# Kernel optimization log

Hardware: AMD Instinct MI355X
Metric: run time of the kernel (lower is better)

## Reference

```python
import jax, jax.numpy as jnp
import numpy as np

A, B, O, ACT, H, NH = 16, 8192, 128, 16, 128, 4
D = H // NH  # attend_dim
IN = O + ACT
NEG = -1e9


def setup_inputs() -> dict:
    key = jax.random.key(0)
    ks = jax.random.split(key, 16)
    s = lambda k, shape, fan: jax.random.normal(k, shape, jnp.float32) / np.sqrt(fan)
    return {
        "obs": jax.random.normal(ks[0], (A, B, O), jnp.float32),
        "actions": jax.random.uniform(ks[1], (A, B, ACT), jnp.float32),
        # per-agent sa-encoder (enc_fc1)
        "W_sa": s(ks[2], (A, IN, H), IN), "b_sa": jnp.zeros((A, H), jnp.float32),
        # per-agent state encoder (s_enc_fc1)
        "W_s": s(ks[3], (A, O, H), O), "b_s": jnp.zeros((A, H), jnp.float32),
        # shared per-head extractors
        "Wk": s(ks[4], (NH, H, D), H),
        "Wsel": s(ks[5], (NH, H, D), H),
        "Wv": s(ks[6], (NH, H, D), H), "bv": jnp.zeros((NH, D), jnp.float32),
        # per-agent critic MLP
        "Wc1": s(ks[7], (A, 2 * H, H), 2 * H), "bc1": jnp.zeros((A, H), jnp.float32),
        "Wc2": s(ks[8], (A, H, ACT), H), "bc2": jnp.zeros((A, ACT), jnp.float32),
    }


def _bn(x):
    # BatchNorm1d(affine=False) in training mode: normalize over batch axis, biased var
    m = x.mean(axis=1, keepdims=True)
    v = x.var(axis=1, keepdims=True)
    return (x - m) / jnp.sqrt(v + 1e-5)


def reference(obs, actions, W_sa, b_sa, W_s, b_s, Wk, Wsel, Wv, bv, Wc1, bc1, Wc2, bc2):
    lrelu = jax.nn.leaky_relu  # slope 0.01, matches torch default
    inp = jnp.concatenate([obs, actions], axis=-1)            # [A,B,IN]
    sa = lrelu(jnp.einsum('abi,aih->abh', _bn(inp), W_sa) + b_sa[:, None, :])  # [A,B,H]
    se = lrelu(jnp.einsum('abo,aoh->abh', _bn(obs), W_s) + b_s[:, None, :])    # [A,B,H]
    keys = jnp.einsum('abh,nhd->nabd', sa, Wk)                # [NH,A,B,D]
    vals = lrelu(jnp.einsum('abh,nhd->nabd', sa, Wv) + bv[:, None, None, :])
    sel = jnp.einsum('abh,nhd->nabd', se, Wsel)
    logits = jnp.einsum('nibd,njbd->nibj', sel, keys) / np.sqrt(D)  # [NH,A,B,A]
    self_mask = jnp.eye(A, dtype=bool)[None, :, None, :]      # mask j == i
    w = jax.nn.softmax(jnp.where(self_mask, NEG, logits), axis=-1)
    other = jnp.einsum('nibj,njbd->nibd', w, vals)            # [NH,A,B,D]
    other = jnp.transpose(other, (1, 2, 0, 3)).reshape(A, B, NH * D)  # head-order concat
    cin = jnp.concatenate([se, other], axis=-1)               # [A,B,2H]
    h = lrelu(jnp.einsum('abk,akh->abh', cin, Wc1) + bc1[:, None, :])
    all_q = jnp.einsum('abh,aho->abo', h, Wc2) + bc2[:, None, :]      # [A,B,ACT]
    idx = jnp.argmax(actions, axis=-1)[..., None]             # int_acs, [A,B,1]
    q = jnp.take_along_axis(all_q, idx, axis=-1)              # [A,B,1]
    return q
```

## Files before the change

### kernel.cpp

```cpp
#include <hip/hip_runtime.h>
#include <hip/hip_bf16.h>

#define A_N 16
#define B_N 8192
#define O_N 128
#define ACT_N 16
#define H_N 128
#define NH_N 4
#define D_N 32
#define IN_N 144
#define NEGV -1e9f

typedef __attribute__((ext_vector_type(8))) short short8;
typedef __attribute__((ext_vector_type(4))) float floatx4;

static __device__ inline unsigned short f2bf(float f) {
    union { float f; unsigned u; } x{f};
    unsigned u = x.u + 0x7FFFu + ((x.u >> 16) & 1u);
    return (unsigned short)(u >> 16);
}
static __device__ inline unsigned pack_bf2(float a, float b) {
    union { float f; unsigned u; } xa{a}, xb{b};
    unsigned ua = xa.u + 0x7FFFu + ((xa.u >> 16) & 1u);
    unsigned ub = xb.u + 0x7FFFu + ((xb.u >> 16) & 1u);
    return (ua >> 16) | (ub & 0xFFFF0000u);
}
static __device__ inline float bf2f(unsigned short h) {
    union { unsigned u; float f; } x;
    x.u = ((unsigned)h) << 16;
    return x.f;
}
static __device__ inline float bflo(unsigned u) {
    union { unsigned u; float f; } x; x.u = u << 16; return x.f;
}
static __device__ inline float bfhi(unsigned u) {
    union { unsigned u; float f; } x; x.u = u & 0xFFFF0000u; return x.f;
}
static __device__ inline short8 ld_frag(const unsigned* p) {
    union { unsigned u[4]; short8 v; } x;
    uint2 lo = *(const uint2*)p;
    uint2 hi = *(const uint2*)(p + 2);
    x.u[0] = lo.x; x.u[1] = lo.y; x.u[2] = hi.x; x.u[3] = hi.y;
    return x.v;
}
static __device__ inline short8 ld_frag4(const unsigned* p) {
    union { uint4 q; short8 v; } x;
    x.q = *(const uint4*)p;
    return x.v;
}

__global__ __launch_bounds__(256) void k_zero(float* p, int n) {
    int i = blockIdx.x * 256 + threadIdx.x;
    if (i < n) p[i] = 0.f;
}

__global__ __launch_bounds__(256) void k_stats(const float* __restrict__ obs,
                                               const float* __restrict__ act,
                                               float* __restrict__ gsum,
                                               float* __restrict__ gsq) {
    __shared__ float ssum[IN_N];
    __shared__ float ssq[IN_N];
    int a = blockIdx.x >> 4;
    int r0 = (blockIdx.x & 15) * 512;
    int t = threadIdx.x;
    if (t < IN_N) { ssum[t] = 0.f; ssq[t] = 0.f; }
    __syncthreads();
    {
        int c0 = (t & 31) * 4, rg = t >> 5;
        const float* p = obs + ((size_t)a * B_N + r0 + rg) * O_N + c0;
        float s0 = 0.f, s1 = 0.f, s2 = 0.f, s3 = 0.f;
        float q0 = 0.f, q1 = 0.f, q2 = 0.f, q3 = 0.f;
#pragma unroll 4
        for (int i = 0; i < 64; ++i) {
            float4 v = *(const float4*)(p + (size_t)i * 8 * O_N);
            s0 += v.x; q0 += v.x * v.x;
            s1 += v.y; q1 += v.y * v.y;
            s2 += v.z; q2 += v.z * v.z;
            s3 += v.w; q3 += v.w * v.w;
        }
        atomicAdd(&ssum[c0 + 0], s0); atomicAdd(&ssq[c0 + 0], q0);
        atomicAdd(&ssum[c0 + 1], s1); atomicAdd(&ssq[c0 + 1], q1);
        atomicAdd(&ssum[c0 + 2], s2); atomicAdd(&ssq[c0 + 2], q2);
        atomicAdd(&ssum[c0 + 3], s3); atomicAdd(&ssq[c0 + 3], q3);
    }
    if (t < 128) {
        int f = t & 15, rg = t >> 4;
        const float* p = act + ((size_t)a * B_N + r0 + rg) * ACT_N + f;
        float s = 0.f, q = 0.f;
#pragma unroll 4
        for (int i = 0; i < 64; ++i) {
            float v = p[(size_t)i * 8 * ACT_N];
            s += v; q += v * v;
        }
        atomicAdd(&ssum[O_N + f], s);
        atomicAdd(&ssq[O_N + f], q);
    }
    __syncthreads();
    if (t < IN_N) {
        atomicAdd(&gsum[a * IN_N + t], ssum[t]);
        atomicAdd(&gsq[a * IN_N + t], ssq[t]);
    }
}

__global__ __launch_bounds__(256) void k_finalize(float* gsum, float* gsq) {
    int i = blockIdx.x * 256 + threadIdx.x;
    if (i < A_N * IN_N) {
        const float invB = 1.f / (float)B_N;
        float m = gsum[i] * invB;
        float v = fmaxf(gsq[i] * invB - m * m, 0.f);
        gsum[i] = m;
        gsq[i] = rsqrtf(v + 1e-5f);
    }
}

#define L1E 393216
#define P1E 409600
#define P2E 417792
#define CRE 679936
#define C2E 712704
__global__ __launch_bounds__(256) void k_wprep(
    const float* __restrict__ W_sa, const float* __restrict__ W_s,
    const float* __restrict__ Wk, const float* __restrict__ Wsel,
    const float* __restrict__ Wv, const float* __restrict__ Wc1,
    const float* __restrict__ Wc2, const float* __restrict__ rstd,
    unsigned* __restrict__ wt_l1, unsigned* __restrict__ wt_p1,
    unsigned* __restrict__ wt_p2, unsigned* __restrict__ wt_cr,
    float* __restrict__ wt_c2) {
    int idx = blockIdx.x * 256 + threadIdx.x;
    if (idx < L1E) {
        int a = idx / 24576, rem = idx % 24576;
        int n = rem & 255, kp = rem >> 8;
        int k0 = 2 * kp, k1 = k0 + 1;
        float v0 = 0.f, v1 = 0.f;
        if (n < 128) {
            if (k0 < IN_N) v0 = W_sa[((size_t)a * IN_N + k0) * H_N + n] * rstd[a * IN_N + k0];
            if (k1 < IN_N) v1 = W_sa[((size_t)a * IN_N + k1) * H_N + n] * rstd[a * IN_N + k1];
        } else {
            int m = n - 128;
            if (k0 < O_N) v0 = W_s[((size_t)a * O_N + k0) * H_N + m] * rstd[a * IN_N + k0];
            if (k1 < O_N) v1 = W_s[((size_t)a * O_N + k1) * H_N + m] * rstd[a * IN_N + k1];
        }
        wt_l1[(size_t)a * 24576 + n * 96 + kp] = pack_bf2(v0, v1);
    } else if (idx < P1E) {
        int i2 = idx - L1E;
        int n = i2 & 255, kp = i2 >> 8;
        int k0 = 2 * kp;
        float v0, v1;
        if (n < 128) {
            const float* w = Wk + ((size_t)(n >> 5) * H_N) * D_N + (n & 31);
            v0 = w[(size_t)k0 * D_N]; v1 = w[(size_t)(k0 + 1) * D_N];
        } else {
            int m = n - 128;
            const float* w = Wv + ((size_t)(m >> 5) * H_N) * D_N + (m & 31);
            v0 = w[(size_t)k0 * D_N]; v1 = w[(size_t)(k0 + 1) * D_N];
        }
        wt_p1[n * 64 + kp] = pack_bf2(v0, v1);
    } else if (idx < P2E) {
        int i3 = idx - P1E;
        int n = i3 & 127, kp = i3 >> 7;
        int k0 = 2 * kp;
        const float* w = Wsel + ((size_t)(n >> 5) * H_N) * D_N + (n & 31);
        wt_p2[n * 64 + kp] = pack_bf2(w[(size_t)k0 * D_N], w[(size_t)(k0 + 1) * D_N]);
    } else if (idx < CRE) {
        int i4 = idx - P2E;
        int a = i4 >> 14, r = i4 & 16383;
        int n = r & 127, kp = r >> 7;
        int k0 = 2 * kp;
        const float* w = Wc1 + (size_t)a * 256 * H_N + n;
        wt_cr[(size_t)a * 16384 + n * 128 + kp] =
            pack_bf2(w[(size_t)k0 * H_N], w[(size_t)(k0 + 1) * H_N]);
    } else if (idx < C2E) {
        int i5 = idx - CRE;
        int a = i5 >> 11, rem = i5 & 2047;
        int oo = rem >> 7, h = rem & 127;
        wt_c2[i5] = Wc2[((size_t)a * H_N + h) * ACT_N + oo];
    }
}

__global__ __launch_bounds__(256) void k_bfold(
    const float* __restrict__ mean, const float* __restrict__ rstd,
    const float* __restrict__ W_sa, const float* __restrict__ W_s,
    const float* __restrict__ b_sa, const float* __restrict__ b_s,
    float* __restrict__ fb) {
    int a = blockIdx.x, c = threadIdx.x;
    float s = 0.f;
    if (c < 128) {
        for (int k = 0; k < IN_N; ++k)
            s += mean[a * IN_N + k] * rstd[a * IN_N + k] *
                 W_sa[((size_t)a * IN_N + k) * H_N + c];
        fb[a * 128 + c] = b_sa[a * H_N + c] - s;
    } else {
        int m = c - 128;
        for (int k = 0; k < O_N; ++k)
            s += mean[a * IN_N + k] * rstd[a * IN_N + k] *
                 W_s[((size_t)a * O_N + k) * H_N + m];
        fb[2048 + a * 128 + m] = b_s[a * H_N + m] - s;
    }
}

__global__ __launch_bounds__(512, 2) void k_l1(
    const float* __restrict__ obs, const float* __restrict__ act,
    const unsigned* __restrict__ wt_l1, const float* __restrict__ fb,
    unsigned short* __restrict__ sa_us, unsigned short* __restrict__ se_us,
    int b0g, int Bc) {
    __shared__ unsigned smem[(128 + 256) * 34];
    unsigned* Xs = smem;
    unsigned* Ws = smem + 128 * 34;

    int a = blockIdx.y;
    int b0 = blockIdx.x * 128;
    int t = threadIdx.x;
    int wid = t >> 6, lane = t & 63, lm = lane & 15, lq = lane >> 4;
    int wrow = (wid & 1) * 64;
    int wcol = (wid >> 1) * 64;

    floatx4 acc[4][4];
#pragma unroll
    for (int mt = 0; mt < 4; ++mt)
#pragma unroll
        for (int nt = 0; nt < 4; ++nt)
#pragma unroll
            for (int e = 0; e < 4; ++e) acc[mt][nt][e] = 0.f;

    const unsigned* WtA = wt_l1 + (size_t)a * 24576;

    for (int c = 0; c < 3; ++c) {
        int kk = c * 64;
        __syncthreads();
        for (int idx = t; idx < 128 * 16; idx += 512) {
            int r = idx >> 4, c4 = idx & 15;
            int k = kk + c4 * 4;
            size_t grow = (size_t)a * B_N + b0g + b0 + r;
            float4 v;
            if (k < O_N) v = *(const float4*)&obs[grow * O_N + k];
            else if (k < IN_N) v = *(const float4*)&act[grow * ACT_N + (k - O_N)];
            else v = make_float4(0.f, 0.f, 0.f, 0.f);
            uint2* dst = (uint2*)&Xs[r * 34 + c4 * 2];
            *dst = make_uint2(pack_bf2(v.x, v.y), pack_bf2(v.z, v.w));
        }
        for (int idx = t; idx < 256 * 8; idx += 512) {
            int n = idx >> 3, c4 = idx & 7;
            uint4 w = *(const uint4*)&WtA[(size_t)n * 96 + (kk >> 1) + c4 * 4];
            uint2* dst = (uint2*)&Ws[n * 34 + c4 * 4];
            dst[0] = make_uint2(w.x, w.y);
            dst[1] = make_uint2(w.z, w.w);
        }
        __syncthreads();
#pragma unroll
        for (int s = 0; s < 2; ++s) {
            if (kk + s * 32 >= 160) break;
            short8 afr[4];
#pragma unroll
            for (int mt = 0; mt < 4; ++mt)
                afr[mt] = ld_frag(&Xs[(wrow + mt * 16 + lm) * 34 + s * 16 + lq * 4]);
#pragma unroll
            for (int nt = 0; nt < 4; ++nt) {
                short8 bfr = ld_frag(&Ws[(wcol + nt * 16 + lm) * 34 + s * 16 + lq * 4]);
#pragma unroll
                for (int mt = 0; mt < 4; ++mt)
                    acc[mt][nt] = __builtin_amdgcn_mfma_f32_16x16x32_bf16(
                        afr[mt], bfr, acc[mt][nt], 0, 0, 0);
            }
        }
    }

    int zsel = (wcol >= 128);
    unsigned short* outp = zsel ? se_us : sa_us;
    const float* bias = fb + zsel * 2048 + a * 128;
    int cbase = wcol & 127;
#pragma unroll
    for (int mt = 0; mt < 4; ++mt)
#pragma unroll
        for (int nt = 0; nt < 4; ++nt)
#pragma unroll
            for (int r = 0; r < 4; ++r) {
                int row = wrow + mt * 16 + lq * 4 + r;
                int col = cbase + nt * 16 + lm;
                float v = acc[mt][nt][r] + bias[col];
                v = v > 0.f ? v : 0.01f * v;
                outp[((size_t)(b0 + row) * 16 + a) * 128 + col] = f2bf(v);
            }
}

__global__ __launch_bounds__(256, 3) void k_fused(
    const unsigned* __restrict__ sa_u, const unsigned* __restrict__ se_u,
    const unsigned* __restrict__ wt_p1, const unsigned* __restrict__ wt_p2,
    const float* __restrict__ bv, unsigned short* __restrict__ other_us,
    int Bc) {
    __shared__ unsigned short keys_s[64 * 130];
    __shared__ unsigned short vals_s[64 * 136];
    __shared__ unsigned short sel_s[64 * 132];

    int bg0 = blockIdx.x * 4;
    int t = threadIdx.x;
    int wid = t >> 6, lane = t & 63, lm = lane & 15, lq = lane >> 4;

    const unsigned* sa_base = sa_u + (size_t)(bg0 * 16) * 64;
    const unsigned* se_base = se_u + (size_t)(bg0 * 16) * 64;

    {
        floatx4 acc[4][4];
#pragma unroll
        for (int mt = 0; mt < 4; ++mt)
#pragma unroll
            for (int nt = 0; nt < 4; ++nt)
#pragma unroll
                for (int e = 0; e < 4; ++e) acc[mt][nt][e] = 0.f;
#pragma unroll
        for (int s = 0; s < 4; ++s) {
            short8 afr[4];
#pragma unroll
            for (int mt = 0; mt < 4; ++mt)
                afr[mt] = ld_frag4(sa_base + (size_t)(mt * 16 + lm) * 64 + s * 16 + lq * 4);
#pragma unroll
            for (int nt = 0; nt < 4; ++nt) {
                int col = wid * 64 + nt * 16 + lm;
                short8 bfr = ld_frag4(wt_p1 + (size_t)col * 64 + s * 16 + lq * 4);
#pragma unroll
                for (int mt = 0; mt < 4; ++mt)
                    acc[mt][nt] = __builtin_amdgcn_mfma_f32_16x16x32_bf16(
                        afr[mt], bfr, acc[mt][nt], 0, 0, 0);
            }
        }
        if (wid < 2) {
#pragma unroll
            for (int mt = 0; mt < 4; ++mt)
#pragma unroll
                for (int nt = 0; nt < 4; ++nt)
#pragma unroll
                    for (int r = 0; r < 4; ++r) {
                        int row = mt * 16 + lq * 4 + r;
                        int col = wid * 64 + nt * 16 + lm;
                        keys_s[row * 130 + col] = f2bf(acc[mt][nt][r]);
                    }
        } else {
#pragma unroll
            for (int mt = 0; mt < 4; ++mt)
#pragma unroll
                for (int nt = 0; nt < 4; ++nt) {
                    int col = (wid - 2) * 64 + nt * 16 + lm;
                    float bvc = bv[col];
#pragma unroll
                    for (int r = 0; r < 4; ++r) {
                        int row = mt * 16 + lq * 4 + r;
                        float v = acc[mt][nt][r] + bvc;
                        v = v > 0.f ? v : 0.01f * v;
                        vals_s[row * 136 + col] = f2bf(v);
                    }
                }
        }
    }
    __syncthreads();

    {
        int wcol = wid * 32;
        floatx4 acc[4][2];
#pragma unroll
        for (int mt = 0; mt < 4; ++mt)
#pragma unroll
            for (int nt = 0; nt < 2; ++nt)
#pragma unroll
                for (int e = 0; e < 4; ++e) acc[mt][nt][e] = 0.f;
#pragma unroll
        for (int s = 0; s < 4; ++s) {
            short8 afr[4];
#pragma unroll
            for (int mt = 0; mt < 4; ++mt)
                afr[mt] = ld_frag4(se_base + (size_t)(mt * 16 + lm) * 64 + s * 16 + lq * 4);
#pragma unroll
            for (int nt = 0; nt < 2; ++nt) {
                int col = wcol + nt * 16 + lm;
                short8 bfr = ld_frag4(wt_p2 + (size_t)col * 64 + s * 16 + lq * 4);
#pragma unroll
                for (int mt = 0; mt < 4; ++mt)
                    acc[mt][nt] = __builtin_amdgcn_mfma_f32_16x16x32_bf16(
                        afr[mt], bfr, acc[mt][nt], 0, 0, 0);
            }
        }
#pragma unroll
        for (int mt = 0; mt < 4; ++mt)
#pragma unroll
            for (int nt = 0; nt < 2; ++nt)
#pragma unroll
                for (int r = 0; r < 4; ++r) {
                    int row = mt * 16 + lq * 4 + r;
                    int col = wcol + nt * 16 + lm;
                    sel_s[row * 132 + col] = f2bf(acc[mt][nt][r]);
                }
    }
    __syncthreads();

    const unsigned* selU = (const unsigned*)sel_s;
    const unsigned* keysU = (const unsigned*)keys_s;
    floatx4 lgacc[4];
#pragma unroll
    for (int n = 0; n < 4; ++n) {
        short8 af = ld_frag(&selU[(wid * 16 + lm) * 66 + n * 16 + lq * 4]);
        short8 bf = ld_frag(&keysU[(wid * 16 + lm) * 65 + n * 16 + lq * 4]);
        floatx4 z4 = {0.f, 0.f, 0.f, 0.f};
        lgacc[n] = __builtin_amdgcn_mfma_f32_16x16x32_bf16(af, bf, z4, 0, 0, 0);
    }
    __syncthreads();

    float* lgs = (float*)keys_s;
#pragma unroll
    for (int n = 0; n < 4; ++n)
#pragma unroll
        for (int r = 0; r < 4; ++r) {
            int i = lq * 4 + r;
            lgs[((wid * 4 + n) * 16 + i) * 16 + lm] =
                lgacc[n][r] * 0.17677669529663687f;
        }
    asm volatile("" ::: "memory");

    int bsub = wid, n = (t >> 4) & 3, i = t & 15;
    float lg[16];
    {
        const float4* lgp = (const float4*)&lgs[((bsub * 4 + n) * 16 + i) * 16];
#pragma unroll
        for (int c = 0; c < 4; ++c) {
            float4 v = lgp[c];
            lg[4 * c] = v.x; lg[4 * c + 1] = v.y;
            lg[4 * c + 2] = v.z; lg[4 * c + 3] = v.w;
        }
    }
    lg[i] = NEGV;
    float m = lg[0];
#pragma unroll
    for (int j = 1; j < 16; ++j) m = fmaxf(m, lg[j]);
    float sum = 0.f;
#pragma unroll
    for (int j = 0; j < 16; ++j) { lg[j] = __expf(lg[j] - m); sum += lg[j]; }
    float inv = 1.f / sum;
#pragma unroll
    for (int j = 0; j < 16; ++j) lg[j] *= inv;

    const unsigned* valsU = (const unsigned*)vals_s;
    float ov[32];
#pragma unroll
    for (int u = 0; u < 32; ++u) ov[u] = 0.f;
#pragma unroll
    for (int j = 0; j < 16; ++j) {
        const uint4* vrow = (const uint4*)&valsU[(bsub * 16 + j) * 68 + n * 16];
        float w = lg[j];
#pragma unroll
        for (int c = 0; c < 4; ++c) {
            uint4 x = vrow[c];
            ov[8 * c + 0] = fmaf(w, bflo(x.x), ov[8 * c + 0]);
            ov[8 * c + 1] = fmaf(w, bfhi(x.x), ov[8 * c + 1]);
            ov[8 * c + 2] = fmaf(w, bflo(x.y), ov[8 * c + 2]);
            ov[8 * c + 3] = fmaf(w, bfhi(x.y), ov[8 * c + 3]);
            ov[8 * c + 4] = fmaf(w, bflo(x.z), ov[8 * c + 4]);
            ov[8 * c + 5] = fmaf(w, bfhi(x.z), ov[8 * c + 5]);
            ov[8 * c + 6] = fmaf(w, bflo(x.w), ov[8 * c + 6]);
            ov[8 * c + 7] = fmaf(w, bfhi(x.w), ov[8 * c + 7]);
        }
    }
    {
        uint4* orow = (uint4*)&other_us[((size_t)(bg0 + bsub) * 16 + i) * 128 + n * 32];
#pragma unroll
        for (int h = 0; h < 2; ++h) {
            uint4 o;
            o.x = pack_bf2(ov[16 * h + 0], ov[16 * h + 1]);
            o.y = pack_bf2(ov[16 * h + 2], ov[16 * h + 3]);
            o.z = pack_bf2(ov[16 * h + 4], ov[16 * h + 5]);
            o.w = pack_bf2(ov[16 * h + 6], ov[16 * h + 7]);
            orow[2 * h] = o;
            o.x = pack_bf2(ov[16 * h + 8], ov[16 * h + 9]);
            o.y = pack_bf2(ov[16 * h + 10], ov[16 * h + 11]);
            o.z = pack_bf2(ov[16 * h + 12], ov[16 * h + 13]);
            o.w = pack_bf2(ov[16 * h + 14], ov[16 * h + 15]);
            orow[2 * h + 1] = o;
        }
    }
}

__global__ __launch_bounds__(256, 4) void k_critic(
    const unsigned* __restrict__ se_u, const unsigned* __restrict__ other_u,
    const unsigned* __restrict__ wt_cr,
    const float* __restrict__ bc1, const float* __restrict__ actions,
    const float* __restrict__ wt_c2, const float* __restrict__ bc2,
    float* __restrict__ qout, int b0g, int Bc) {
    __shared__ unsigned smem[(64 + 128) * 34];
    unsigned* Xs = smem;
    unsigned* Ws = smem + 64 * 34;

    int a = blockIdx.y;
    int b0 = blockIdx.x * 64;
    int t = threadIdx.x;
    int wid = t >> 6, lane = t & 63, lm = lane & 15, lq = lane >> 4;
    int wrow = (wid & 1) * 32;
    int wcol = (wid >> 1) * 64;

    floatx4 acc[2][4];
#pragma unroll
    for (int mt = 0; mt < 2; ++mt)
#pragma unroll
        for (int nt = 0; nt < 4; ++nt)
#pragma unroll
            for (int e = 0; e < 4; ++e) acc[mt][nt][e] = 0.f;

    const unsigned* WtA = wt_cr + (size_t)a * 16384;

    for (int c = 0; c < 4; ++c) {
        int kk = c * 64;
        __syncthreads();
        const unsigned* src = (c < 2) ? se_u : other_u;
        int off = (c & 1) * 32;
        for (int idx = t; idx < 64 * 8; idx += 256) {
            int r = idx >> 3, c4 = idx & 7;
            uint4 v = *(const uint4*)&src[((size_t)(b0 + r) * 16 + a) * 64 + off + c4 * 4];
            uint2* dst = (uint2*)&Xs[r * 34 + c4 * 4];
            dst[0] = make_uint2(v.x, v.y);
            dst[1] = make_uint2(v.z, v.w);
        }
        for (int idx = t; idx < 128 * 8; idx += 256) {
            int n = idx >> 3, c4 = idx & 7;
            uint4 w = *(const uint4*)&WtA[(size_t)n * 128 + (kk >> 1) + c4 * 4];
            uint2* dst = (uint2*)&Ws[n * 34 + c4 * 4];
            dst[0] = make_uint2(w.x, w.y);
            dst[1] = make_uint2(w.z, w.w);
        }
        __syncthreads();
#pragma unroll
        for (int s = 0; s < 2; ++s) {
            short8 afr[2];
#pragma unroll
            for (int mt = 0; mt < 2; ++mt)
                afr[mt] = ld_frag(&Xs[(wrow + mt * 16 + lm) * 34 + s * 16 + lq * 4]);
#pragma unroll
            for (int nt = 0; nt < 4; ++nt) {
                short8 bfr = ld_frag(&Ws[(wcol + nt * 16 + lm) * 34 + s * 16 + lq * 4]);
#pragma unroll
                for (int mt = 0; mt < 2; ++mt)
                    acc[mt][nt] = __builtin_amdgcn_mfma_f32_16x16x32_bf16(
                        afr[mt], bfr, acc[mt][nt], 0, 0, 0);
            }
        }
    }

    __syncthreads();
    unsigned short* hbuf = (unsigned short*)smem;
#pragma unroll
    for (int mt = 0; mt < 2; ++mt)
#pragma unroll
        for (int nt = 0; nt < 4; ++nt)
#pragma unroll
            for (int r = 0; r < 4; ++r) {
                int row = wrow + mt * 16 + lq * 4 + r;
                int col = wcol + nt * 16 + lm;
                float v = acc[mt][nt][r] + bc1[a * H_N + col];
                v = v > 0.f ? v : 0.01f * v;
                hbuf[row * 132 + col] = f2bf(v);
            }
    __syncthreads();
    if (t < 64) {
        size_t arow = (size_t)a * B_N + b0g + b0 + t;
        const float* ap = &actions[arow * ACT_N];
        float bestv = ap[0];
        int bi = 0;
        for (int o = 1; o < ACT_N; ++o) {
            float v = ap[o];
            if (v > bestv) { bestv = v; bi = o; }
        }
        float q = bc2[a * ACT_N + bi];
        const float4* w4p = (const float4*)&wt_c2[((size_t)a * ACT_N + bi) * H_N];
        const uint2* hp2 = (const uint2*)&hbuf[t * 132];
#pragma unroll
        for (int h4 = 0; h4 < 32; ++h4) {
            float4 w4 = w4p[h4];
            uint2 hh = hp2[h4];
            q = fmaf(bflo(hh.x), w4.x, q);
            q = fmaf(bfhi(hh.x), w4.y, q);
            q = fmaf(bflo(hh.y), w4.z, q);
            q = fmaf(bfhi(hh.y), w4.w, q);
        }
        qout[arow] = q;
    }
}

extern "C" void kernel_launch(void* const* d_in, const int* in_sizes, int n_in,
                              void* d_out, int out_size, void* d_ws, size_t ws_size,
                              hipStream_t stream) {
    const float* obs     = (const float*)d_in[0];
    const float* actions = (const float*)d_in[1];
    const float* W_sa    = (const float*)d_in[2];
    const float* b_sa    = (const float*)d_in[3];
    const float* W_s     = (const float*)d_in[4];
    const float* b_s     = (const float*)d_in[5];
    const float* Wk      = (const float*)d_in[6];
    const float* Wsel    = (const float*)d_in[7];
    const float* Wv      = (const float*)d_in[8];
    const float* bv      = (const float*)d_in[9];
    const float* Wc1     = (const float*)d_in[10];
    const float* bc1     = (const float*)d_in[11];
    const float* Wc2     = (const float*)d_in[12];
    const float* bc2     = (const float*)d_in[13];
    float* out = (float*)d_out;
    char* ws = (char*)d_ws;

    size_t o = 0;
    float* gsum = (float*)(ws + o); o += 2304 * 4;
    float* gsq  = (float*)(ws + o); o += 2304 * 4;
    unsigned* wt_l1 = (unsigned*)(ws + o); o += (size_t)393216 * 4;
    unsigned* wt_p1 = (unsigned*)(ws + o); o += (size_t)16384 * 4;
    unsigned* wt_p2 = (unsigned*)(ws + o); o += (size_t)8192 * 4;
    unsigned* wt_cr = (unsigned*)(ws + o); o += (size_t)262144 * 4;
    float* fb = (float*)(ws + o); o += (size_t)4096 * 4;
    float* wt_c2 = (float*)(ws + o); o += (size_t)32768 * 4;
    size_t fixed = o;

    int Bc = B_N;
    while (Bc > 128 && fixed + 12288ull * Bc > ws_size) Bc >>= 1;

    unsigned short* sa_us = (unsigned short*)(ws + o); o += (size_t)A_N * Bc * 128 * 2;
    unsigned short* se_us = (unsigned short*)(ws + o); o += (size_t)A_N * Bc * 128 * 2;
    unsigned short* ot_us = (unsigned short*)(ws + o); o += (size_t)A_N * Bc * 128 * 2;

    k_zero<<<dim3(18), 256, 0, stream>>>(gsum, 2 * A_N * IN_N);
    k_stats<<<dim3(A_N * 16), 256, 0, stream>>>(obs, actions, gsum, gsq);
    k_finalize<<<dim3(9), 256, 0, stream>>>(gsum, gsq);
    k_wprep<<<dim3(C2E / 256), 256, 0, stream>>>(W_sa, W_s, Wk, Wsel, Wv, Wc1, Wc2,
                                                 gsq, wt_l1, wt_p1, wt_p2, wt_cr, wt_c2);
    k_bfold<<<dim3(A_N), 256, 0, stream>>>(gsum, gsq, W_sa, W_s, b_sa, b_s, fb);

    for (int b0g = 0; b0g < B_N; b0g += Bc) {
        k_l1<<<dim3(Bc / 128, A_N), 512, 0, stream>>>(
            obs, actions, wt_l1, fb, sa_us, se_us, b0g, Bc);
        k_fused<<<dim3(Bc / 4), 256, 0, stream>>>(
            (const unsigned*)sa_us, (const unsigned*)se_us, wt_p1, wt_p2, bv,
            ot_us, Bc);
        k_critic<<<dim3(Bc / 64, A_N), 256, 0, stream>>>(
            (const unsigned*)se_us, (const unsigned*)ot_us, wt_cr, bc1,
            actions, wt_c2, bc2, out, b0g, Bc);
    }
}
```

Baseline: 299.4 us.

## Drop zero/bfold launches, stage tiles in LDS, move attention softmax-V onto MFMA

```diff
diff --git a/kernel.cpp b/kernel.cpp
--- a/kernel.cpp
+++ b/kernel.cpp
@@ -49,19 +49,15 @@
     return x.v;
 }
 
-__global__ __launch_bounds__(256) void k_zero(float* p, int n) {
-    int i = blockIdx.x * 256 + threadIdx.x;
-    if (i < n) p[i] = 0.f;
-}
-
 __global__ __launch_bounds__(256) void k_stats(const float* __restrict__ obs,
                                                const float* __restrict__ act,
-                                               float* __restrict__ gsum,
-                                               float* __restrict__ gsq) {
+                                               float* __restrict__ gsumP,
+                                               float* __restrict__ gsqP) {
     __shared__ float ssum[IN_N];
     __shared__ float ssq[IN_N];
     int a = blockIdx.x >> 4;
-    int r0 = (blockIdx.x & 15) * 512;
+    int slab = blockIdx.x & 15;
+    int r0 = slab * 512;
     int t = threadIdx.x;
     if (t < IN_N) { ssum[t] = 0.f; ssq[t] = 0.f; }
     __syncthreads();
@@ -97,19 +93,29 @@
     }
     __syncthreads();
     if (t < IN_N) {
-        atomicAdd(&gsum[a * IN_N + t], ssum[t]);
-        atomicAdd(&gsq[a * IN_N + t], ssq[t]);
-    }
-}
-
-__global__ __launch_bounds__(256) void k_finalize(float* gsum, float* gsq) {
+        gsumP[(a * 16 + slab) * IN_N + t] = ssum[t];
+        gsqP[(a * 16 + slab) * IN_N + t] = ssq[t];
+    }
+}
+
+__global__ __launch_bounds__(256) void k_finalize(const float* __restrict__ gsumP,
+                                                  const float* __restrict__ gsqP,
+                                                  float* __restrict__ mean,
+                                                  float* __restrict__ rstd) {
     int i = blockIdx.x * 256 + threadIdx.x;
     if (i < A_N * IN_N) {
+        int a = i / IN_N, f = i - a * IN_N;
+        float s = 0.f, q = 0.f;
+#pragma unroll
+        for (int sl = 0; sl < 16; ++sl) {
+            s += gsumP[(a * 16 + sl) * IN_N + f];
+            q += gsqP[(a * 16 + sl) * IN_N + f];
+        }
         const float invB = 1.f / (float)B_N;
-        float m = gsum[i] * invB;
-        float v = fmaxf(gsq[i] * invB - m * m, 0.f);
-        gsum[i] = m;
-        gsq[i] = rsqrtf(v + 1e-5f);
+        float m = s * invB;
+        float v = fmaxf(q * invB - m * m, 0.f);
+        mean[i] = m;
+        rstd[i] = rsqrtf(v + 1e-5f);
     }
 }
 
@@ -118,14 +124,17 @@
 #define P2E 417792
 #define CRE 679936
 #define C2E 712704
+#define BFE (C2E + 4096)
 __global__ __launch_bounds__(256) void k_wprep(
     const float* __restrict__ W_sa, const float* __restrict__ W_s,
     const float* __restrict__ Wk, const float* __restrict__ Wsel,
     const float* __restrict__ Wv, const float* __restrict__ Wc1,
-    const float* __restrict__ Wc2, const float* __restrict__ rstd,
+    const float* __restrict__ Wc2, const float* __restrict__ mean,
+    const float* __restrict__ rstd,
+    const float* __restrict__ b_sa, const float* __restrict__ b_s,
     unsigned* __restrict__ wt_l1, unsigned* __restrict__ wt_p1,
     unsigned* __restrict__ wt_p2, unsigned* __restrict__ wt_cr,
-    float* __restrict__ wt_c2) {
+    float* __restrict__ wt_c2, float* __restrict__ fb) {
     int idx = blockIdx.x * 256 + threadIdx.x;
     if (idx < L1E) {
         int a = idx / 24576, rem = idx % 24576;
@@ -174,27 +183,22 @@
         int a = i5 >> 11, rem = i5 & 2047;
         int oo = rem >> 7, h = rem & 127;
         wt_c2[i5] = Wc2[((size_t)a * H_N + h) * ACT_N + oo];
-    }
-}
-
-__global__ __launch_bounds__(256) void k_bfold(
-    const float* __restrict__ mean, const float* __restrict__ rstd,
-    const float* __restrict__ W_sa, const float* __restrict__ W_s,
-    const float* __restrict__ b_sa, const float* __restrict__ b_s,
-    float* __restrict__ fb) {
-    int a = blockIdx.x, c = threadIdx.x;
-    float s = 0.f;
-    if (c < 128) {
-        for (int k = 0; k < IN_N; ++k)
-            s += mean[a * IN_N + k] * rstd[a * IN_N + k] *
-                 W_sa[((size_t)a * IN_N + k) * H_N + c];
-        fb[a * 128 + c] = b_sa[a * H_N + c] - s;
-    } else {
-        int m = c - 128;
-        for (int k = 0; k < O_N; ++k)
-            s += mean[a * IN_N + k] * rstd[a * IN_N + k] *
-                 W_s[((size_t)a * O_N + k) * H_N + m];
-        fb[2048 + a * 128 + m] = b_s[a * H_N + m] - s;
+    } else if (idx < BFE) {
+        int i6 = idx - C2E;
+        int a = i6 >> 8, c = i6 & 255;
+        float s = 0.f;
+        if (c < 128) {
+            for (int k = 0; k < IN_N; ++k)
+                s += mean[a * IN_N + k] * rstd[a * IN_N + k] *
+                     W_sa[((size_t)a * IN_N + k) * H_N + c];
+            fb[a * 128 + c] = b_sa[a * H_N + c] - s;
+        } else {
+            int m = c - 128;
+            for (int k = 0; k < O_N; ++k)
+                s += mean[a * IN_N + k] * rstd[a * IN_N + k] *
+                     W_s[((size_t)a * O_N + k) * H_N + m];
+            fb[2048 + a * 128 + m] = b_s[a * H_N + m] - s;
+        }
     }
 }
 
@@ -287,9 +291,10 @@
     const unsigned* __restrict__ wt_p1, const unsigned* __restrict__ wt_p2,
     const float* __restrict__ bv, unsigned short* __restrict__ other_us,
     int Bc) {
+    __shared__ unsigned Xs[64 * 66];
     __shared__ unsigned short keys_s[64 * 130];
-    __shared__ unsigned short vals_s[64 * 136];
-    __shared__ unsigned short sel_s[64 * 132];
+    __shared__ unsigned short valsT[4 * 128 * 16];
+    unsigned short* sel_s = (unsigned short*)Xs;
 
     int bg0 = blockIdx.x * 4;
     int t = threadIdx.x;
@@ -298,6 +303,19 @@
     const unsigned* sa_base = sa_u + (size_t)(bg0 * 16) * 64;
     const unsigned* se_base = se_u + (size_t)(bg0 * 16) * 64;
 
+    for (int idx = t; idx < 64 * 16; idx += 256) {
+        int r = idx >> 4, c4 = idx & 15;
+        uint4 v = *(const uint4*)&sa_base[(size_t)idx * 4];
+        uint2* dst = (uint2*)&Xs[r * 66 + c4 * 4];
+        dst[0] = make_uint2(v.x, v.y);
+        dst[1] = make_uint2(v.z, v.w);
+    }
+    uint4 seR[4];
+#pragma unroll
+    for (int ii = 0; ii < 4; ++ii)
+        seR[ii] = *(const uint4*)&se_base[(size_t)(t + ii * 256) * 4];
+    __syncthreads();
+
     {
         floatx4 acc[4][4];
 #pragma unroll
@@ -311,7 +329,7 @@
             short8 afr[4];
 #pragma unroll
             for (int mt = 0; mt < 4; ++mt)
-                afr[mt] = ld_frag4(sa_base + (size_t)(mt * 16 + lm) * 64 + s * 16 + lq * 4);
+                afr[mt] = ld_frag(&Xs[(mt * 16 + lm) * 66 + s * 16 + lq * 4]);
 #pragma unroll
             for (int nt = 0; nt < 4; ++nt) {
                 int col = wid * 64 + nt * 16 + lm;
@@ -338,17 +356,26 @@
             for (int mt = 0; mt < 4; ++mt)
 #pragma unroll
                 for (int nt = 0; nt < 4; ++nt) {
-                    int col = (wid - 2) * 64 + nt * 16 + lm;
-                    float bvc = bv[col];
-#pragma unroll
-                    for (int r = 0; r < 4; ++r) {
-                        int row = mt * 16 + lq * 4 + r;
-                        float v = acc[mt][nt][r] + bvc;
-                        v = v > 0.f ? v : 0.01f * v;
-                        vals_s[row * 136 + col] = f2bf(v);
-                    }
+                    int d = (wid - 2) * 64 + nt * 16 + lm;
+                    float bvc = bv[d];
+                    float v0 = acc[mt][nt][0] + bvc; v0 = v0 > 0.f ? v0 : 0.01f * v0;
+                    float v1 = acc[mt][nt][1] + bvc; v1 = v1 > 0.f ? v1 : 0.01f * v1;
+                    float v2 = acc[mt][nt][2] + bvc; v2 = v2 > 0.f ? v2 : 0.01f * v2;
+                    float v3 = acc[mt][nt][3] + bvc; v3 = v3 > 0.f ? v3 : 0.01f * v3;
+                    uint2 o = make_uint2(pack_bf2(v0, v1), pack_bf2(v2, v3));
+                    *(uint2*)&valsT[mt * 2048 + d * 16 + lq * 4] = o;
                 }
         }
+    }
+    __syncthreads();
+
+#pragma unroll
+    for (int ii = 0; ii < 4; ++ii) {
+        int idx = t + ii * 256;
+        int r = idx >> 4, c4 = idx & 15;
+        uint2* dst = (uint2*)&Xs[r * 66 + c4 * 4];
+        dst[0] = make_uint2(seR[ii].x, seR[ii].y);
+        dst[1] = make_uint2(seR[ii].z, seR[ii].w);
     }
     __syncthreads();
 
@@ -366,7 +393,7 @@
             short8 afr[4];
 #pragma unroll
             for (int mt = 0; mt < 4; ++mt)
-                afr[mt] = ld_frag4(se_base + (size_t)(mt * 16 + lm) * 64 + s * 16 + lq * 4);
+                afr[mt] = ld_frag(&Xs[(mt * 16 + lm) * 66 + s * 16 + lq * 4]);
 #pragma unroll
             for (int nt = 0; nt < 2; ++nt) {
                 int col = wcol + nt * 16 + lm;
@@ -377,6 +404,7 @@
                         afr[mt], bfr, acc[mt][nt], 0, 0, 0);
             }
         }
+        __syncthreads();
 #pragma unroll
         for (int mt = 0; mt < 4; ++mt)
 #pragma unroll
@@ -392,85 +420,71 @@
 
     const unsigned* selU = (const unsigned*)sel_s;
     const unsigned* keysU = (const unsigned*)keys_s;
+    int bsub = wid;
     floatx4 lgacc[4];
 #pragma unroll
     for (int n = 0; n < 4; ++n) {
-        short8 af = ld_frag(&selU[(wid * 16 + lm) * 66 + n * 16 + lq * 4]);
-        short8 bf = ld_frag(&keysU[(wid * 16 + lm) * 65 + n * 16 + lq * 4]);
+        short8 af = ld_frag(&keysU[(bsub * 16 + lm) * 65 + n * 16 + lq * 4]);
+        short8 bf = ld_frag(&selU[(bsub * 16 + lm) * 66 + n * 16 + lq * 4]);
         floatx4 z4 = {0.f, 0.f, 0.f, 0.f};
         lgacc[n] = __builtin_amdgcn_mfma_f32_16x16x32_bf16(af, bf, z4, 0, 0, 0);
     }
-    __syncthreads();
-
-    float* lgs = (float*)keys_s;
-#pragma unroll
-    for (int n = 0; n < 4; ++n)
-#pragma unroll
-        for (int r = 0; r < 4; ++r) {
-            int i = lq * 4 + r;
-            lgs[((wid * 4 + n) * 16 + i) * 16 + lm] =
-                lgacc[n][r] * 0.17677669529663687f;
-        }
-    asm volatile("" ::: "memory");
-
-    int bsub = wid, n = (t >> 4) & 3, i = t & 15;
-    float lg[16];
-    {
-        const float4* lgp = (const float4*)&lgs[((bsub * 4 + n) * 16 + i) * 16];
-#pragma unroll
-        for (int c = 0; c < 4; ++c) {
-            float4 v = lgp[c];
-            lg[4 * c] = v.x; lg[4 * c + 1] = v.y;
-            lg[4 * c + 2] = v.z; lg[4 * c + 3] = v.w;
-        }
-    }
-    lg[i] = NEGV;
-    float m = lg[0];
-#pragma unroll
-    for (int j = 1; j < 16; ++j) m = fmaxf(m, lg[j]);
-    float sum = 0.f;
-#pragma unroll
-    for (int j = 0; j < 16; ++j) { lg[j] = __expf(lg[j] - m); sum += lg[j]; }
-    float inv = 1.f / sum;
-#pragma unroll
-    for (int j = 0; j < 16; ++j) lg[j] *= inv;
-
-    const unsigned* valsU = (const unsigned*)vals_s;
-    float ov[32];
-#pragma unroll
-    for (int u = 0; u < 32; ++u) ov[u] = 0.f;
-#pragma unroll
-    for (int j = 0; j < 16; ++j) {
-        const uint4* vrow = (const uint4*)&valsU[(bsub * 16 + j) * 68 + n * 16];
-        float w = lg[j];
-#pragma unroll
-        for (int c = 0; c < 4; ++c) {
-            uint4 x = vrow[c];
-            ov[8 * c + 0] = fmaf(w, bflo(x.x), ov[8 * c + 0]);
-            ov[8 * c + 1] = fmaf(w, bfhi(x.x), ov[8 * c + 1]);
-            ov[8 * c + 2] = fmaf(w, bflo(x.y), ov[8 * c + 2]);
-            ov[8 * c + 3] = fmaf(w, bfhi(x.y), ov[8 * c + 3]);
-            ov[8 * c + 4] = fmaf(w, bflo(x.z), ov[8 * c + 4]);
-            ov[8 * c + 5] = fmaf(w, bfhi(x.z), ov[8 * c + 5]);
-            ov[8 * c + 6] = fmaf(w, bflo(x.w), ov[8 * c + 6]);
-            ov[8 * c + 7] = fmaf(w, bfhi(x.w), ov[8 * c + 7]);
-        }
-    }
-    {
-        uint4* orow = (uint4*)&other_us[((size_t)(bg0 + bsub) * 16 + i) * 128 + n * 32];
-#pragma unroll
-        for (int h = 0; h < 2; ++h) {
-            uint4 o;
-            o.x = pack_bf2(ov[16 * h + 0], ov[16 * h + 1]);
-            o.y = pack_bf2(ov[16 * h + 2], ov[16 * h + 3]);
-            o.z = pack_bf2(ov[16 * h + 4], ov[16 * h + 5]);
-            o.w = pack_bf2(ov[16 * h + 6], ov[16 * h + 7]);
-            orow[2 * h] = o;
-            o.x = pack_bf2(ov[16 * h + 8], ov[16 * h + 9]);
-            o.y = pack_bf2(ov[16 * h + 10], ov[16 * h + 11]);
-            o.z = pack_bf2(ov[16 * h + 12], ov[16 * h + 13]);
-            o.w = pack_bf2(ov[16 * h + 14], ov[16 * h + 15]);
-            orow[2 * h + 1] = o;
+
+    const float scale = 0.17677669529663687f;
+    int dr = lm - lq * 4;
+    unsigned pq0[4], pq1[4];
+#pragma unroll
+    for (int n = 0; n < 4; ++n) {
+        float p0 = lgacc[n][0] * scale;
+        float p1 = lgacc[n][1] * scale;
+        float p2 = lgacc[n][2] * scale;
+        float p3 = lgacc[n][3] * scale;
+        if (dr == 0) p0 = NEGV;
+        if (dr == 1) p1 = NEGV;
+        if (dr == 2) p2 = NEGV;
+        if (dr == 3) p3 = NEGV;
+        float m = fmaxf(fmaxf(p0, p1), fmaxf(p2, p3));
+        m = fmaxf(m, __shfl_xor(m, 16));
+        m = fmaxf(m, __shfl_xor(m, 32));
+        p0 = __expf(p0 - m); p1 = __expf(p1 - m);
+        p2 = __expf(p2 - m); p3 = __expf(p3 - m);
+        float s = p0 + p1 + p2 + p3;
+        s += __shfl_xor(s, 16);
+        s += __shfl_xor(s, 32);
+        float inv = 1.f / s;
+        pq0[n] = pack_bf2(p0 * inv, p1 * inv);
+        pq1[n] = pack_bf2(p2 * inv, p3 * inv);
+    }
+
+    const unsigned* valsTU = (const unsigned*)valsT;
+    int g = lq & 1;
+    int s0l = (g << 5) + lm;
+    int s1l = s0l + 16;
+    size_t obase = ((size_t)(bg0 + bsub) * 16 + lm) * 128;
+#pragma unroll
+    for (int n = 0; n < 4; ++n) {
+        unsigned b0 = __shfl(pq0[n], s0l);
+        unsigned b1 = __shfl(pq1[n], s0l);
+        unsigned b2 = __shfl(pq0[n], s1l);
+        unsigned b3 = __shfl(pq1[n], s1l);
+        if (lq >= 2) { b0 = 0u; b1 = 0u; b2 = 0u; b3 = 0u; }
+        short8 bfr;
+        {
+            union { unsigned u[4]; short8 v; } x;
+            x.u[0] = b0; x.u[1] = b1; x.u[2] = b2; x.u[3] = b3;
+            bfr = x.v;
+        }
+#pragma unroll
+        for (int dt = 0; dt < 2; ++dt) {
+            int d = n * 32 + dt * 16 + lm;
+            uint4 av = *(const uint4*)(valsTU + ((bsub << 10) + d * 8 + (g << 2)));
+            if (lq >= 2) { av.x = 0u; av.y = 0u; av.z = 0u; av.w = 0u; }
+            short8 afr;
+            { union { uint4 q; short8 v; } x; x.q = av; afr = x.v; }
+            floatx4 z4 = {0.f, 0.f, 0.f, 0.f};
+            floatx4 c = __builtin_amdgcn_mfma_f32_16x16x32_bf16(afr, bfr, z4, 0, 0, 0);
+            uint2 o = make_uint2(pack_bf2(c[0], c[1]), pack_bf2(c[2], c[3]));
+            *(uint2*)&other_us[obase + n * 32 + dt * 16 + lq * 4] = o;
         }
     }
 }
@@ -600,8 +614,10 @@
     char* ws = (char*)d_ws;
 
     size_t o = 0;
-    float* gsum = (float*)(ws + o); o += 2304 * 4;
-    float* gsq  = (float*)(ws + o); o += 2304 * 4;
+    float* gsumP = (float*)(ws + o); o += (size_t)36864 * 4;
+    float* gsqP  = (float*)(ws + o); o += (size_t)36864 * 4;
+    float* meanA = (float*)(ws + o); o += 2304 * 4;
+    float* rstdA = (float*)(ws + o); o += 2304 * 4;
     unsigned* wt_l1 = (unsigned*)(ws + o); o += (size_t)393216 * 4;
     unsigned* wt_p1 = (unsigned*)(ws + o); o += (size_t)16384 * 4;
     unsigned* wt_p2 = (unsigned*)(ws + o); o += (size_t)8192 * 4;
@@ -617,12 +633,11 @@
     unsigned short* se_us = (unsigned short*)(ws + o); o += (size_t)A_N * Bc * 128 * 2;
     unsigned short* ot_us = (unsigned short*)(ws + o); o += (size_t)A_N * Bc * 128 * 2;
 
-    k_zero<<<dim3(18), 256, 0, stream>>>(gsum, 2 * A_N * IN_N);
-    k_stats<<<dim3(A_N * 16), 256, 0, stream>>>(obs, actions, gsum, gsq);
-    k_finalize<<<dim3(9), 256, 0, stream>>>(gsum, gsq);
-    k_wprep<<<dim3(C2E / 256), 256, 0, stream>>>(W_sa, W_s, Wk, Wsel, Wv, Wc1, Wc2,
-                                                 gsq, wt_l1, wt_p1, wt_p2, wt_cr, wt_c2);
-    k_bfold<<<dim3(A_N), 256, 0, stream>>>(gsum, gsq, W_sa, W_s, b_sa, b_s, fb);
+    k_stats<<<dim3(A_N * 16), 256, 0, stream>>>(obs, actions, gsumP, gsqP);
+    k_finalize<<<dim3(9), 256, 0, stream>>>(gsumP, gsqP, meanA, rstdA);
+    k_wprep<<<dim3(BFE / 256), 256, 0, stream>>>(W_sa, W_s, Wk, Wsel, Wv, Wc1, Wc2,
+                                                 meanA, rstdA, b_sa, b_s,
+                                                 wt_l1, wt_p1, wt_p2, wt_cr, wt_c2, fb);
 
     for (int b0g = 0; b0g < B_N; b0g += Bc) {
         k_l1<<<dim3(Bc / 128, A_N), 512, 0, stream>>>(
```

After: 266.6 us. -11.0%, faster.
